# Optimization experiments

Hardware: AMD Instinct MI355X
Metric: run time of the kernel (lower is better)

## Reference

```python
import jax, jax.numpy as jnp
import numpy as np

EMBED_DIM = 768
NUM_HEADS = 12
HEAD_DIM = EMBED_DIM // NUM_HEADS


def setup_inputs() -> dict:
    key = jax.random.key(0)
    k_x, k_wqkv, k_bqkv, k_wo, k_bo = jax.random.split(key, 5)
    B, S = 2, 4096
    x = jax.random.normal(k_x, (B, S, EMBED_DIM), dtype=jnp.float32)
    # nn.Linear default init: U(-1/sqrt(fan_in), 1/sqrt(fan_in))
    bound = 1.0 / np.sqrt(EMBED_DIM)
    w_qkv = jax.random.uniform(k_wqkv, (EMBED_DIM, 3 * EMBED_DIM), jnp.float32, -bound, bound)
    b_qkv = jax.random.uniform(k_bqkv, (3 * EMBED_DIM,), jnp.float32, -bound, bound)
    w_out = jax.random.uniform(k_wo, (EMBED_DIM, EMBED_DIM), jnp.float32, -bound, bound)
    b_out = jax.random.uniform(k_bo, (EMBED_DIM,), jnp.float32, -bound, bound)
    return {"x": x, "w_qkv": w_qkv, "b_qkv": b_qkv, "w_out": w_out, "b_out": b_out}


def reference(x, w_qkv, b_qkv, w_out, b_out):
    B, S, E = x.shape
    H, D = NUM_HEADS, HEAD_DIM
    qkv = x @ w_qkv + b_qkv                       # [B,S,3E]
    qkv = qkv.reshape(B, S, 3, H, D)
    q = qkv[:, :, 0].transpose(0, 2, 1, 3)        # [B,H,S,D]
    k = qkv[:, :, 1].transpose(0, 2, 1, 3)
    v = qkv[:, :, 2].transpose(0, 2, 1, 3)
    scores = jnp.einsum('bhqd,bhkd->bhqk', q, k) / jnp.sqrt(jnp.float32(D))
    causal = jnp.tril(jnp.ones((S, S), dtype=bool))
    scores = jnp.where(causal, scores, -jnp.inf)
    weights = jax.nn.softmax(scores, axis=-1)
    attended = jnp.einsum('bhqk,bhkd->bhqd', weights, v)  # [B,H,S,D]
    attended = attended.transpose(0, 2, 1, 3).reshape(B, S, E)
    return attended @ w_out + b_out
```

## Files before the change

### kernel.cpp

```cpp
#include <hip/hip_runtime.h>

#define EMBED 768
#define NH 12
#define HD 64
#define SEQ 4096
#define BATCH 2
#define MROWS (BATCH * SEQ)
#define N3E (3 * EMBED)

typedef short bf16x8 __attribute__((ext_vector_type(8)));
typedef float fx4 __attribute__((ext_vector_type(4)));
typedef float f32x16 __attribute__((ext_vector_type(16)));
typedef unsigned short ushort_t;
typedef unsigned short us4 __attribute__((ext_vector_type(4)));

#if __has_builtin(__builtin_amdgcn_exp2f)
#define EXP2F(x) __builtin_amdgcn_exp2f(x)
#else
#define EXP2F(x) exp2f(x)
#endif

#define QSCALE 0.18033688011112042f

__device__ inline ushort_t f2bf(float f) {
  union { float f; unsigned int u; } x; x.f = f;
  unsigned int r = x.u + 0x7fffu + ((x.u >> 16) & 1u);
  return (ushort_t)(r >> 16);
}

__device__ inline unsigned int cvtpk(float a, float b) {
  unsigned int r;
  asm("v_cvt_pk_bf16_f32 %0, %1, %2" : "=v"(r) : "v"(a), "v"(b));
  return r;
}

__device__ inline void plswap(unsigned int& x, unsigned int& y) {
  asm("v_permlane32_swap_b32 %0, %1" : "+v"(x), "+v"(y));
}

__global__ __launch_bounds__(256) void convert_x(const float* __restrict__ in,
                                                 ushort_t* __restrict__ out) {
  int i = (blockIdx.x * 256 + threadIdx.x) * 8;
  float4 a = *(const float4*)(in + i);
  float4 b = *(const float4*)(in + i + 4);
  bf16x8 o;
  o[0] = f2bf(a.x); o[1] = f2bf(a.y); o[2] = f2bf(a.z); o[3] = f2bf(a.w);
  o[4] = f2bf(b.x); o[5] = f2bf(b.y); o[6] = f2bf(b.z); o[7] = f2bf(b.w);
  *(bf16x8*)(out + i) = o;
}

__global__ __launch_bounds__(256) void transpose_w(const float* __restrict__ in,
                                                   ushort_t* __restrict__ out,
                                                   int K, int N) {
  __shared__ float t[64][65];
  const int bn = blockIdx.x * 64, bk = blockIdx.y * 64;
  const int c = threadIdx.x & 63, r0 = threadIdx.x >> 6;
#pragma unroll
  for (int rr = 0; rr < 16; ++rr) {
    int row = rr * 4 + r0;
    t[row][c] = in[(size_t)(bk + row) * N + bn + c];
  }
  __syncthreads();
#pragma unroll
  for (int rr = 0; rr < 16; ++rr) {
    int row = rr * 4 + r0;
    out[(size_t)(bn + row) * K + bk + c] = f2bf(t[c][row]);
  }
}

template <int N_, int K_, bool SCATTER>
__global__ __launch_bounds__(256) void gemm_mfma(
    const ushort_t* __restrict__ A, const ushort_t* __restrict__ Bt,
    const float* __restrict__ bias, float* __restrict__ outF,
    ushort_t* __restrict__ oq, ushort_t* __restrict__ ok,
    ushort_t* __restrict__ ov) {
  __shared__ __align__(16) ushort_t As[128 * 32];
  __shared__ __align__(16) ushort_t Bs[128 * 32];
  const int tid = threadIdx.x;
  const int w = tid >> 6, lane = tid & 63;
  const int quad = lane >> 4, ln = lane & 15;
  const int bm = blockIdx.y * 128, bn = blockIdx.x * 128;
  const int wm = (w >> 1) * 64, wn = (w & 1) * 64;

  const int sr = lane >> 2;
  const int sslot = lane & 3;

  fx4 acc[4][4] = {};

  for (int k0 = 0; k0 < K_; k0 += 32) {
    __syncthreads();
#pragma unroll
    for (int r = 0; r < 2; ++r) {
      const int c = w + r * 4;
      const int m = c * 16 + sr;
      const int kk = k0 + ((sslot ^ (m & 3)) << 3);
      __builtin_amdgcn_global_load_lds(
          (const __attribute__((address_space(1))) unsigned int*)
              (A + (size_t)(bm + m) * K_ + kk),
          (__attribute__((address_space(3))) unsigned int*)(As + c * 512),
          16, 0, 0);
      __builtin_amdgcn_global_load_lds(
          (const __attribute__((address_space(1))) unsigned int*)
              (Bt + (size_t)(bn + m) * K_ + kk),
          (__attribute__((address_space(3))) unsigned int*)(Bs + c * 512),
          16, 0, 0);
    }
    __syncthreads();

    bf16x8 af[4], bfr[4];
#pragma unroll
    for (int i = 0; i < 4; ++i) {
      const int m = wm + i * 16 + ln;
      af[i] = *(const bf16x8*)(As + m * 32 + ((quad ^ (m & 3)) << 3));
    }
#pragma unroll
    for (int j = 0; j < 4; ++j) {
      const int n = wn + j * 16 + ln;
      bfr[j] = *(const bf16x8*)(Bs + n * 32 + ((quad ^ (n & 3)) << 3));
    }
#pragma unroll
    for (int i = 0; i < 4; ++i)
#pragma unroll
      for (int j = 0; j < 4; ++j)
        acc[i][j] = __builtin_amdgcn_mfma_f32_16x16x32_bf16(af[i], bfr[j],
                                                            acc[i][j], 0, 0, 0);
  }

  if (!SCATTER) {
#pragma unroll
    for (int j = 0; j < 4; ++j) {
      const int n = bn + wn + j * 16 + ln;
      const float bv = bias[n];
#pragma unroll
      for (int i = 0; i < 4; ++i) {
        const int m0 = bm + wm + i * 16 + quad * 4;
#pragma unroll
        for (int r = 0; r < 4; ++r)
          outF[(size_t)(m0 + r) * N_ + n] = acc[i][j][r] + bv;
      }
    }
  } else {
    const int t = bn / EMBED;
#pragma unroll
    for (int j = 0; j < 4; ++j) {
      const int nn = bn + wn + j * 16 + ln;
      const int rem = nn - t * EMBED;
      const int h = rem >> 6, d = rem & 63;
      const float bv = bias[nn];
#pragma unroll
      for (int i = 0; i < 4; ++i) {
        const int m0 = bm + wm + i * 16 + quad * 4;
#pragma unroll
        for (int r = 0; r < 4; ++r) {
          const int m = m0 + r;
          const int b_ = m >> 12, s = m & 4095;
          const float v = acc[i][j][r] + bv;
          if (t == 0)
            oq[((size_t)(b_ * NH + h) * SEQ + s) * HD + d] = f2bf(v * QSCALE);
          else if (t == 1)
            ok[((size_t)(b_ * NH + h) * SEQ + s) * HD + d] = f2bf(v);
          else
            ov[((size_t)(b_ * NH + h) * HD + d) * SEQ + s] = f2bf(v);
        }
      }
    }
  }
}

__global__ __launch_bounds__(128, 3) void flash_mfma(
    const ushort_t* __restrict__ qb, const ushort_t* __restrict__ kb,
    const ushort_t* __restrict__ vb, ushort_t* __restrict__ attn) {
  __shared__ __align__(16) ushort_t Ks[2][64 * 64];
  __shared__ __align__(16) ushort_t Vt[2][64 * 64];

  const int tid = threadIdx.x;
  const int w = tid >> 6;
  const int lane = tid & 63;
  const int r32 = lane & 31;
  const int hf = lane >> 5;
  const int gk = r32 & 7;
  const int rc4 = hf * 4;

  const int bh = blockIdx.x;
  const int qt = 63 - (int)blockIdx.y;
  const int nkt = qt + 1;

  const size_t base = (size_t)bh * SEQ * HD;
  const ushort_t* Qg = qb + base;
  const ushort_t* Kg = kb + base;
  const ushort_t* Vg = vb + base;

  const int srow = lane >> 3;
  const int sg = (lane & 7) ^ srow;
  const int row0 = w * 8 + srow;
  const ushort_t* kp = Kg + (size_t)row0 * HD + (sg << 3);
  const ushort_t* vp = Vg + (size_t)row0 * SEQ + (sg << 3);

  const int qoff = w * 32 + r32;
  const int qglob = qt * 64 + qoff;
  bf16x8 qf[4];
  {
    const ushort_t* qrow = Qg + (size_t)qglob * HD;
#pragma unroll
    for (int dc = 0; dc < 4; ++dc)
      qf[dc] = *(const bf16x8*)(qrow + dc * 16 + hf * 8);
  }

  f32x16 oacc[2] = {};
  float lsum = 0.f;

#pragma unroll
  for (int r2 = 0; r2 < 4; ++r2) {
    __builtin_amdgcn_global_load_lds(
        (const __attribute__((address_space(1))) unsigned int*)(kp + r2 * (16 * HD)),
        (__attribute__((address_space(3))) unsigned int*)(&Ks[0][(w + r2 * 2) * 512]),
        16, 0, 0);
    __builtin_amdgcn_global_load_lds(
        (const __attribute__((address_space(1))) unsigned int*)(vp + r2 * (16 * SEQ)),
        (__attribute__((address_space(3))) unsigned int*)(&Vt[0][(w + r2 * 2) * 512]),
        16, 0, 0);
  }
  kp += 64 * HD;
  vp += 64;

  for (int kt = 0; kt < nkt; ++kt) {
    const int cur = kt & 1;
    __syncthreads();
    if (kt + 1 < nkt) {
      const int nxt = cur ^ 1;
#pragma unroll
      for (int r2 = 0; r2 < 4; ++r2) {
        __builtin_amdgcn_global_load_lds(
            (const __attribute__((address_space(1))) unsigned int*)(kp + r2 * (16 * HD)),
            (__attribute__((address_space(3))) unsigned int*)(&Ks[nxt][(w + r2 * 2) * 512]),
            16, 0, 0);
        __builtin_amdgcn_global_load_lds(
            (const __attribute__((address_space(1))) unsigned int*)(vp + r2 * (16 * SEQ)),
            (__attribute__((address_space(3))) unsigned int*)(&Vt[nxt][(w + r2 * 2) * 512]),
            16, 0, 0);
      }
      kp += 64 * HD;
      vp += 64;
    }

    const bool diag = (kt == nkt - 1);

#pragma unroll
    for (int krb = 0; krb < 2; ++krb) {
      if (diag && krb > w) continue;
      const int krow = (krb * 32 + r32) * 64;
      f32x16 s = {};
#pragma unroll
      for (int dc = 0; dc < 4; ++dc) {
        bf16x8 kf =
            *(const bf16x8*)(&Ks[cur][krow + (((2 * dc + hf) ^ gk) << 3)]);
        s = __builtin_amdgcn_mfma_f32_32x32x16_bf16(kf, qf[dc], s, 0, 0, 0);
      }
      if (diag && krb == w) {
#pragma unroll
        for (int r = 0; r < 16; ++r) {
          const int rowc = (r & 3) + 8 * (r >> 2) + rc4;
          if (rowc > r32) s[r] = -1e30f;
        }
      }
      float e[16];
#pragma unroll
      for (int r = 0; r < 16; ++r) {
        e[r] = EXP2F(s[r]);
        lsum += e[r];
      }
#pragma unroll
      for (int ch = 0; ch < 2; ++ch) {
        const int rb = ch * 8;
        unsigned int x0 = cvtpk(e[rb + 0], e[rb + 1]);
        unsigned int x1 = cvtpk(e[rb + 2], e[rb + 3]);
        unsigned int y0 = cvtpk(e[rb + 4], e[rb + 5]);
        unsigned int y1 = cvtpk(e[rb + 6], e[rb + 7]);
        plswap(x0, y0);
        plswap(x1, y1);
        union { unsigned int u[4]; bf16x8 v; } pf;
        pf.u[0] = x0; pf.u[1] = x1; pf.u[2] = y0; pf.u[3] = y1;
        const int c = 2 * krb + ch;
        __builtin_amdgcn_s_setprio(1);
#pragma unroll
        for (int vb2 = 0; vb2 < 2; ++vb2) {
          const int vrow = (vb2 * 32 + r32) * 64;
          bf16x8 vf =
              *(const bf16x8*)(&Vt[cur][vrow + (((2 * c + hf) ^ gk) << 3)]);
          oacc[vb2] =
              __builtin_amdgcn_mfma_f32_32x32x16_bf16(vf, pf.v, oacc[vb2], 0, 0, 0);
        }
        __builtin_amdgcn_s_setprio(0);
      }
    }
  }

  lsum += __shfl_xor(lsum, 32);
  const float inv = 1.f / lsum;
  const int b_ = bh / NH, h = bh % NH;
  ushort_t* orow = attn + (size_t)(b_ * SEQ + qglob) * EMBED + h * HD;
#pragma unroll
  for (int vb2 = 0; vb2 < 2; ++vb2)
#pragma unroll
    for (int rq = 0; rq < 4; ++rq) {
      us4 o;
#pragma unroll
      for (int r = 0; r < 4; ++r) o[r] = f2bf(oacc[vb2][rq * 4 + r] * inv);
      *(us4*)(orow + vb2 * 32 + rq * 8 + rc4) = o;
    }
}

extern "C" void kernel_launch(void* const* d_in, const int* in_sizes, int n_in,
                              void* d_out, int out_size, void* d_ws,
                              size_t ws_size, hipStream_t stream) {
  const float* x = (const float*)d_in[0];
  const float* w_qkv = (const float*)d_in[1];
  const float* b_qkv = (const float*)d_in[2];
  const float* w_out = (const float*)d_in[3];
  const float* b_out = (const float*)d_in[4];
  float* out = (float*)d_out;

  const size_t per = (size_t)BATCH * NH * SEQ * HD;
  ushort_t* q_buf = (ushort_t*)d_ws;
  ushort_t* k_buf = q_buf + per;
  ushort_t* v_buf = k_buf + per;
  ushort_t* attn_buf = v_buf + per;
  ushort_t* xb = attn_buf + per;
  ushort_t* wqkvT = xb + per;
  ushort_t* woutT = wqkvT + (size_t)N3E * EMBED;

  convert_x<<<(MROWS * EMBED) / 2048, 256, 0, stream>>>(x, xb);
  transpose_w<<<dim3(N3E / 64, EMBED / 64), 256, 0, stream>>>(w_qkv, wqkvT,
                                                              EMBED, N3E);
  transpose_w<<<dim3(EMBED / 64, EMBED / 64), 256, 0, stream>>>(w_out, woutT,
                                                                EMBED, EMBED);

  dim3 g1(N3E / 128, MROWS / 128);
  gemm_mfma<N3E, EMBED, true><<<g1, 256, 0, stream>>>(
      xb, wqkvT, b_qkv, nullptr, q_buf, k_buf, v_buf);

  dim3 g2(BATCH * NH, 64);
  flash_mfma<<<g2, 128, 0, stream>>>(q_buf, k_buf, v_buf, attn_buf);

  dim3 g3(EMBED / 128, MROWS / 128);
  gemm_mfma<EMBED, EMBED, false><<<g3, 256, 0, stream>>>(
      attn_buf, woutT, b_out, out, nullptr, nullptr, nullptr);
}
```

Measured before the change: 257.7 us.

## Restructure flash attention to one wave handling both 32-row query halves

```diff
diff --git a/kernel.cpp b/kernel.cpp
--- a/kernel.cpp
+++ b/kernel.cpp
@@ -167,146 +167,178 @@
   }
 }
 
-__global__ __launch_bounds__(128, 3) void flash_mfma(
+__global__ __launch_bounds__(64, 2) void flash_mfma(
     const ushort_t* __restrict__ qb, const ushort_t* __restrict__ kb,
     const ushort_t* __restrict__ vb, ushort_t* __restrict__ attn) {
-  __shared__ __align__(16) ushort_t Ks[2][64 * 64];
-  __shared__ __align__(16) ushort_t Vt[2][64 * 64];
-
-  const int tid = threadIdx.x;
-  const int w = tid >> 6;
-  const int lane = tid & 63;
+  __shared__ __align__(16) ushort_t Ks[2][32 * 64];
+  __shared__ __align__(16) ushort_t Vt[2][64 * 32];
+
+  const int lane = threadIdx.x;
   const int r32 = lane & 31;
   const int hf = lane >> 5;
   const int gk = r32 & 7;
+  const int gv = (r32 >> 1) & 3;
   const int rc4 = hf * 4;
 
   const int bh = blockIdx.x;
-  const int qt = 63 - (int)blockIdx.y;
-  const int nkt = qt + 1;
+  const int p = 63 - (int)blockIdx.y;
+  const int kend = 2 * p + 1;
 
   const size_t base = (size_t)bh * SEQ * HD;
   const ushort_t* Qg = qb + base;
   const ushort_t* Kg = kb + base;
   const ushort_t* Vg = vb + base;
 
-  const int srow = lane >> 3;
-  const int sg = (lane & 7) ^ srow;
-  const int row0 = w * 8 + srow;
-  const ushort_t* kp = Kg + (size_t)row0 * HD + (sg << 3);
-  const ushort_t* vp = Vg + (size_t)row0 * SEQ + (sg << 3);
-
-  const int qoff = w * 32 + r32;
-  const int qglob = qt * 64 + qoff;
-  bf16x8 qf[4];
+  const int krow_s = lane >> 3;
+  const int kg_s = (lane & 7) ^ krow_s;
+  const int vrow_s = lane >> 2;
+  const int vg_s = (lane & 3) ^ ((vrow_s >> 1) & 3);
+  const ushort_t* kbase[4];
+  const ushort_t* vbase[4];
+#pragma unroll
+  for (int i = 0; i < 4; ++i) {
+    kbase[i] = Kg + i * 512 + krow_s * 64 + kg_s * 8;
+    vbase[i] = Vg + (size_t)(16 * i + vrow_s) * SEQ + vg_s * 8;
+  }
+
+  int koff[4], voff[4];
+#pragma unroll
+  for (int dc = 0; dc < 4; ++dc)
+    koff[dc] = r32 * 64 + (((2 * dc + hf) ^ gk) << 3);
+#pragma unroll
+  for (int vb2 = 0; vb2 < 2; ++vb2)
+#pragma unroll
+    for (int ch = 0; ch < 2; ++ch)
+      voff[vb2 * 2 + ch] =
+          (vb2 * 32 + r32) * 32 + (((2 * ch + hf) ^ gv) << 3);
+
+  bf16x8 qfA[4], qfB[4];
   {
-    const ushort_t* qrow = Qg + (size_t)qglob * HD;
+    const ushort_t* qra = Qg + (size_t)(64 * p + r32) * HD;
+    const ushort_t* qrb = qra + 32 * HD;
+#pragma unroll
+    for (int dc = 0; dc < 4; ++dc) {
+      qfA[dc] = *(const bf16x8*)(qra + dc * 16 + hf * 8);
+      qfB[dc] = *(const bf16x8*)(qrb + dc * 16 + hf * 8);
+    }
+  }
+
+  auto STAGE = [&](int ks, int buf) {
+#pragma unroll
+    for (int i = 0; i < 4; ++i) {
+      __builtin_amdgcn_global_load_lds(
+          (const __attribute__((address_space(1))) unsigned int*)
+              (kbase[i] + (size_t)ks * 2048),
+          (__attribute__((address_space(3))) unsigned int*)(&Ks[buf][i * 512]),
+          16, 0, 0);
+      __builtin_amdgcn_global_load_lds(
+          (const __attribute__((address_space(1))) unsigned int*)
+              (vbase[i] + ks * 32),
+          (__attribute__((address_space(3))) unsigned int*)(&Vt[buf][i * 512]),
+          16, 0, 0);
+    }
+  };
+
+  f32x16 oA0 = {}, oA1 = {}, oB0 = {}, oB1 = {};
+  float lA = 0.f, lB = 0.f;
+
+  auto smpv = [&](f32x16 s, float& lsum, f32x16& o0, f32x16& o1, bool dg,
+                  const bf16x8 (&vf)[4]) {
+    if (dg) {
+#pragma unroll
+      for (int r = 0; r < 16; ++r) {
+        const int rowc = (r & 3) + 8 * (r >> 2) + rc4;
+        if (rowc > r32) s[r] = -1e30f;
+      }
+    }
+    float e[16];
+#pragma unroll
+    for (int r = 0; r < 16; ++r) e[r] = EXP2F(s[r]);
+    {
+      float t0 = ((e[0] + e[1]) + (e[2] + e[3])) +
+                 ((e[4] + e[5]) + (e[6] + e[7]));
+      float t1 = ((e[8] + e[9]) + (e[10] + e[11])) +
+                 ((e[12] + e[13]) + (e[14] + e[15]));
+      lsum += t0 + t1;
+    }
+    bf16x8 pf[2];
+#pragma unroll
+    for (int ch = 0; ch < 2; ++ch) {
+      const int rb = ch * 8;
+      unsigned int x0 = cvtpk(e[rb + 0], e[rb + 1]);
+      unsigned int x1 = cvtpk(e[rb + 2], e[rb + 3]);
+      unsigned int y0 = cvtpk(e[rb + 4], e[rb + 5]);
+      unsigned int y1 = cvtpk(e[rb + 6], e[rb + 7]);
+      plswap(x0, y0);
+      plswap(x1, y1);
+      union { unsigned int u[4]; bf16x8 v; } w_;
+      w_.u[0] = x0; w_.u[1] = x1; w_.u[2] = y0; w_.u[3] = y1;
+      pf[ch] = w_.v;
+    }
+    __builtin_amdgcn_s_setprio(1);
+    o0 = __builtin_amdgcn_mfma_f32_32x32x16_bf16(vf[0], pf[0], o0, 0, 0, 0);
+    o1 = __builtin_amdgcn_mfma_f32_32x32x16_bf16(vf[2], pf[0], o1, 0, 0, 0);
+    o0 = __builtin_amdgcn_mfma_f32_32x32x16_bf16(vf[1], pf[1], o0, 0, 0, 0);
+    o1 = __builtin_amdgcn_mfma_f32_32x32x16_bf16(vf[3], pf[1], o1, 0, 0, 0);
+    __builtin_amdgcn_s_setprio(0);
+  };
+
+  STAGE(0, 0);
+  STAGE(1, 1);
+
+  for (int kt = 0; kt <= kend; ++kt) {
+    const int cur = kt & 1;
+    asm volatile("s_waitcnt vmcnt(8)" ::: "memory");
+    bf16x8 kf[4], vf[4];
 #pragma unroll
     for (int dc = 0; dc < 4; ++dc)
-      qf[dc] = *(const bf16x8*)(qrow + dc * 16 + hf * 8);
-  }
-
-  f32x16 oacc[2] = {};
-  float lsum = 0.f;
-
-#pragma unroll
-  for (int r2 = 0; r2 < 4; ++r2) {
-    __builtin_amdgcn_global_load_lds(
-        (const __attribute__((address_space(1))) unsigned int*)(kp + r2 * (16 * HD)),
-        (__attribute__((address_space(3))) unsigned int*)(&Ks[0][(w + r2 * 2) * 512]),
-        16, 0, 0);
-    __builtin_amdgcn_global_load_lds(
-        (const __attribute__((address_space(1))) unsigned int*)(vp + r2 * (16 * SEQ)),
-        (__attribute__((address_space(3))) unsigned int*)(&Vt[0][(w + r2 * 2) * 512]),
-        16, 0, 0);
-  }
-  kp += 64 * HD;
-  vp += 64;
-
-  for (int kt = 0; kt < nkt; ++kt) {
-    const int cur = kt & 1;
-    __syncthreads();
-    if (kt + 1 < nkt) {
-      const int nxt = cur ^ 1;
-#pragma unroll
-      for (int r2 = 0; r2 < 4; ++r2) {
-        __builtin_amdgcn_global_load_lds(
-            (const __attribute__((address_space(1))) unsigned int*)(kp + r2 * (16 * HD)),
-            (__attribute__((address_space(3))) unsigned int*)(&Ks[nxt][(w + r2 * 2) * 512]),
-            16, 0, 0);
-        __builtin_amdgcn_global_load_lds(
-            (const __attribute__((address_space(1))) unsigned int*)(vp + r2 * (16 * SEQ)),
-            (__attribute__((address_space(3))) unsigned int*)(&Vt[nxt][(w + r2 * 2) * 512]),
-            16, 0, 0);
-      }
-      kp += 64 * HD;
-      vp += 64;
-    }
-
-    const bool diag = (kt == nkt - 1);
-
-#pragma unroll
-    for (int krb = 0; krb < 2; ++krb) {
-      if (diag && krb > w) continue;
-      const int krow = (krb * 32 + r32) * 64;
-      f32x16 s = {};
+      kf[dc] = *(const bf16x8*)(&Ks[cur][koff[dc]]);
+#pragma unroll
+    for (int j = 0; j < 4; ++j)
+      vf[j] = *(const bf16x8*)(&Vt[cur][voff[j]]);
+
+    if (kt < kend) {
+      f32x16 sA = {}, sB = {};
 #pragma unroll
       for (int dc = 0; dc < 4; ++dc) {
-        bf16x8 kf =
-            *(const bf16x8*)(&Ks[cur][krow + (((2 * dc + hf) ^ gk) << 3)]);
-        s = __builtin_amdgcn_mfma_f32_32x32x16_bf16(kf, qf[dc], s, 0, 0, 0);
-      }
-      if (diag && krb == w) {
-#pragma unroll
-        for (int r = 0; r < 16; ++r) {
-          const int rowc = (r & 3) + 8 * (r >> 2) + rc4;
-          if (rowc > r32) s[r] = -1e30f;
-        }
-      }
-      float e[16];
-#pragma unroll
-      for (int r = 0; r < 16; ++r) {
-        e[r] = EXP2F(s[r]);
-        lsum += e[r];
-      }
-#pragma unroll
-      for (int ch = 0; ch < 2; ++ch) {
-        const int rb = ch * 8;
-        unsigned int x0 = cvtpk(e[rb + 0], e[rb + 1]);
-        unsigned int x1 = cvtpk(e[rb + 2], e[rb + 3]);
-        unsigned int y0 = cvtpk(e[rb + 4], e[rb + 5]);
-        unsigned int y1 = cvtpk(e[rb + 6], e[rb + 7]);
-        plswap(x0, y0);
-        plswap(x1, y1);
-        union { unsigned int u[4]; bf16x8 v; } pf;
-        pf.u[0] = x0; pf.u[1] = x1; pf.u[2] = y0; pf.u[3] = y1;
-        const int c = 2 * krb + ch;
-        __builtin_amdgcn_s_setprio(1);
-#pragma unroll
-        for (int vb2 = 0; vb2 < 2; ++vb2) {
-          const int vrow = (vb2 * 32 + r32) * 64;
-          bf16x8 vf =
-              *(const bf16x8*)(&Vt[cur][vrow + (((2 * c + hf) ^ gk) << 3)]);
-          oacc[vb2] =
-              __builtin_amdgcn_mfma_f32_32x32x16_bf16(vf, pf.v, oacc[vb2], 0, 0, 0);
-        }
-        __builtin_amdgcn_s_setprio(0);
-      }
-    }
-  }
-
-  lsum += __shfl_xor(lsum, 32);
-  const float inv = 1.f / lsum;
+        sB = __builtin_amdgcn_mfma_f32_32x32x16_bf16(kf[dc], qfB[dc], sB, 0, 0, 0);
+        sA = __builtin_amdgcn_mfma_f32_32x32x16_bf16(kf[dc], qfA[dc], sA, 0, 0, 0);
+      }
+      smpv(sA, lA, oA0, oA1, kt == kend - 1, vf);
+      smpv(sB, lB, oB0, oB1, false, vf);
+    } else {
+      f32x16 sB = {};
+#pragma unroll
+      for (int dc = 0; dc < 4; ++dc)
+        sB = __builtin_amdgcn_mfma_f32_32x32x16_bf16(kf[dc], qfB[dc], sB, 0, 0, 0);
+      smpv(sB, lB, oB0, oB1, true, vf);
+    }
+
+    asm volatile("s_waitcnt lgkmcnt(0)" ::: "memory");
+    __builtin_amdgcn_sched_barrier(0);
+    const int ks = (kt + 2 <= kend) ? (kt + 2) : kend;
+    STAGE(ks, cur);
+  }
+
+  lA += __shfl_xor(lA, 32);
+  lB += __shfl_xor(lB, 32);
+  const float invA = 1.f / lA;
+  const float invB = 1.f / lB;
   const int b_ = bh / NH, h = bh % NH;
-  ushort_t* orow = attn + (size_t)(b_ * SEQ + qglob) * EMBED + h * HD;
+  ushort_t* orA = attn + (size_t)(b_ * SEQ + 64 * p + r32) * EMBED + h * HD;
+  ushort_t* orB = orA + (size_t)32 * EMBED;
 #pragma unroll
   for (int vb2 = 0; vb2 < 2; ++vb2)
 #pragma unroll
     for (int rq = 0; rq < 4; ++rq) {
-      us4 o;
-#pragma unroll
-      for (int r = 0; r < 4; ++r) o[r] = f2bf(oacc[vb2][rq * 4 + r] * inv);
-      *(us4*)(orow + vb2 * 32 + rq * 8 + rc4) = o;
+      us4 oa, ob;
+#pragma unroll
+      for (int r = 0; r < 4; ++r) {
+        oa[r] = f2bf((vb2 ? oA1 : oA0)[rq * 4 + r] * invA);
+        ob[r] = f2bf((vb2 ? oB1 : oB0)[rq * 4 + r] * invB);
+      }
+      *(us4*)(orA + vb2 * 32 + rq * 8 + rc4) = oa;
+      *(us4*)(orB + vb2 * 32 + rq * 8 + rc4) = ob;
     }
 }
 
@@ -340,7 +372,7 @@
       xb, wqkvT, b_qkv, nullptr, q_buf, k_buf, v_buf);
 
   dim3 g2(BATCH * NH, 64);
-  flash_mfma<<<g2, 128, 0, stream>>>(q_buf, k_buf, v_buf, attn_buf);
+  flash_mfma<<<g2, 64, 0, stream>>>(q_buf, k_buf, v_buf, attn_buf);
 
   dim3 g3(EMBED / 128, MROWS / 128);
   gemm_mfma<EMBED, EMBED, false><<<g3, 256, 0, stream>>>(
```

New measurement: 301.8 us. 1.17x slower.
